# Kernel optimization log

Hardware: AMD Instinct MI355X
Metric: run time of the kernel (lower is better)

## Reference

```python
import jax, jax.numpy as jnp
import numpy as np

E = 128  # embedding_dim
C = 32   # per-head dim
H = 4    # heads
L = 256  # seq_len
N = 1    # batch


def layer_norm(x, gamma, beta, eps=1e-5):
    mu = jnp.mean(x, axis=-1, keepdims=True)
    var = jnp.mean((x - mu) ** 2, axis=-1, keepdims=True)
    return (x - mu) * jax.lax.rsqrt(var + eps) * gamma + beta


def setup_inputs() -> dict:
    key = jax.random.key(0)
    ks = jax.random.split(key, 12)
    s = E ** -0.5
    return {
        "pair_rep": jax.random.normal(ks[0], (N, L, L, E), dtype=jnp.float32),
        "mask": jax.random.normal(ks[1], (N, L, L), dtype=jnp.float32) * 0.1,
        "gamma": jnp.ones((E,), dtype=jnp.float32),
        "beta": jnp.zeros((E,), dtype=jnp.float32),
        "Wq": jax.random.normal(ks[2], (E, C * H), dtype=jnp.float32) * s,
        "Wk": jax.random.normal(ks[3], (E, C * H), dtype=jnp.float32) * s,
        "Wv": jax.random.normal(ks[4], (E, C * H), dtype=jnp.float32) * s,
        "Wb": jax.random.normal(ks[5], (E, H), dtype=jnp.float32) * s,
        "Wfu": jax.random.normal(ks[6], (E, C * H), dtype=jnp.float32) * s,
        "bfu": jnp.zeros((C * H,), dtype=jnp.float32),
        "Wo": jax.random.normal(ks[7], (C * H, E), dtype=jnp.float32) * (C * H) ** -0.5,
        "bo": jnp.zeros((E,), dtype=jnp.float32),
    }


def reference(pair_rep, mask, gamma, beta, Wq, Wk, Wv, Wb, Wfu, bfu, Wo, bo):
    n, s, _, _ = pair_rep.shape
    x = layer_norm(pair_rep, gamma, beta)  # [n,s,s,E]
    q = (x @ Wq).reshape(n, s, s, H, C) * (C ** -0.5)
    k = (x @ Wk).reshape(n, s, s, H, C)
    v = (x @ Wv).reshape(n, s, s, H, C)
    # faithful to original einsum: keys carry the q index, queries the v index
    dpa = jnp.einsum('nsqhc,nsvhc->nsqvh', k, q)  # [n,s,q,v,h]
    dpa = dpa + mask[:, None, :, :, None]
    pair_bias = x @ Wb  # [n,s,s,H]
    attn = jax.nn.softmax(dpa + pair_bias[:, None], axis=3)
    out = jnp.einsum('nsqvh,nsvhc->nsqhc', attn, v)  # [n,s,q,h,c]
    fu = jax.nn.sigmoid(x @ Wfu + bfu).reshape(n, s, s, H, C)
    out = out * fu
    out = out.reshape(n, s, s, H * C) @ Wo + bo
    return out
```

## Files before the change

### kernel.cpp

```cpp
#include <hip/hip_runtime.h>
#include <math.h>

#define L 256
#define E 128
#define H 4
#define C 32
#define P (L*L)

typedef __bf16 bf16;
typedef __bf16 bf16x8 __attribute__((ext_vector_type(8)));
typedef __bf16 bf16x4 __attribute__((ext_vector_type(4)));
typedef float  f32x4  __attribute__((ext_vector_type(4)));

#define MFMA(a,b,c) __builtin_amdgcn_mfma_f32_16x16x32_bf16((a),(b),(c),0,0,0)

__global__ __launch_bounds__(256) void k_prep(
    const float* __restrict__ Wq, const float* __restrict__ Wk,
    const float* __restrict__ Wv, const float* __restrict__ Wfu,
    const float* __restrict__ Wo, const float* __restrict__ Wb,
    bf16* __restrict__ WF, bf16* __restrict__ WoF, bf16* __restrict__ WbF)
{
  const int b = blockIdx.x;
  const int lane = threadIdx.x & 63, wv = threadIdx.x >> 6;
  const int g = lane >> 4, l15 = lane & 15;
  if (b < 40) {
    const int m = b >> 3;
    const int f = (b & 7) * 4 + wv;
    const float* W = (m==0)?Wq:(m==1)?Wk:(m==2)?Wv:(m==3)?Wfu:Wo;
    bf16* dst = (m < 4) ? (WF + (size_t)m * 16384) : WoF;
    const float sc = (m == 0) ? 0.17677669529663689f : 1.0f;
    const int mt = f >> 2, kt = f & 3;
    const int row = 16*mt + l15, k0 = 32*kt + 8*g;
    bf16x8 o;
    #pragma unroll
    for (int j = 0; j < 8; ++j) o[j] = (bf16)(W[(size_t)(k0+j)*128 + row] * sc);
    *(bf16x8*)(dst + ((size_t)f*64 + lane)*8) = o;
  } else {
    const int kt = wv, k0 = 32*kt + 8*g;
    bf16x8 o;
    #pragma unroll
    for (int j = 0; j < 8; ++j)
      o[j] = (l15 < 4) ? (bf16)Wb[(size_t)(k0+j)*4 + l15] : (bf16)0.0f;
    *(bf16x8*)(WbF + ((size_t)kt*64 + lane)*8) = o;
  }
}

__global__ __launch_bounds__(512) void k_ln_proj(
    const float* __restrict__ pr, const float* __restrict__ gamma,
    const float* __restrict__ beta, const float* __restrict__ bfu,
    const bf16* __restrict__ WF, const bf16* __restrict__ WbF,
    bf16* __restrict__ qbh, bf16* __restrict__ kbh, bf16* __restrict__ vbh,
    bf16* __restrict__ gfb, float* __restrict__ pbo)
{
  __shared__ bf16 xs[64 * 136];
  __shared__ bf16 stag[4][16 * 136];
  const int tid = threadIdx.x;
  const int base = blockIdx.x * 64;
  const int w = tid >> 6, lane = tid & 63, g = lane >> 4, l15 = lane & 15;
  const int m = w & 3, half = w >> 2;

  const bf16* WFw = WF + (size_t)m * 16384 + (size_t)half * 8192;
  f32x4 af[16];
  #pragma unroll
  for (int f = 0; f < 16; ++f)
    af[f] = *(const f32x4*)(WFw + ((size_t)f*64 + lane)*8);

  {
    const int pl = tid >> 3, sub = tid & 7;
    const float4* src = (const float4*)(pr + (size_t)(base + pl) * 128 + sub * 16);
    float4 r[4];
    float s = 0.f, ss = 0.f;
    #pragma unroll
    for (int j = 0; j < 4; ++j) {
      r[j] = src[j];
      s  += r[j].x + r[j].y + r[j].z + r[j].w;
      ss += r[j].x*r[j].x + r[j].y*r[j].y + r[j].z*r[j].z + r[j].w*r[j].w;
    }
    s  += __shfl_xor(s, 1, 8);  s  += __shfl_xor(s, 2, 8);  s  += __shfl_xor(s, 4, 8);
    ss += __shfl_xor(ss, 1, 8); ss += __shfl_xor(ss, 2, 8); ss += __shfl_xor(ss, 4, 8);
    const float mu   = s * 0.0078125f;
    const float var  = ss * 0.0078125f - mu * mu;
    const float rstd = rsqrtf(var + 1e-5f);
    const float4* g4 = (const float4*)(gamma + sub * 16);
    const float4* b4 = (const float4*)(beta + sub * 16);
    bf16* xr = xs + pl * 136 + sub * 16;
    #pragma unroll
    for (int i = 0; i < 2; ++i) {
      float4 r0 = r[2*i], r1 = r[2*i+1];
      float4 gg0 = g4[2*i], gg1 = g4[2*i+1], bb0 = b4[2*i], bb1 = b4[2*i+1];
      bf16x8 o;
      o[0] = (bf16)((r0.x - mu) * rstd * gg0.x + bb0.x);
      o[1] = (bf16)((r0.y - mu) * rstd * gg0.y + bb0.y);
      o[2] = (bf16)((r0.z - mu) * rstd * gg0.z + bb0.z);
      o[3] = (bf16)((r0.w - mu) * rstd * gg0.w + bb0.w);
      o[4] = (bf16)((r1.x - mu) * rstd * gg1.x + bb1.x);
      o[5] = (bf16)((r1.y - mu) * rstd * gg1.y + bb1.y);
      o[6] = (bf16)((r1.z - mu) * rstd * gg1.z + bb1.z);
      o[7] = (bf16)((r1.w - mu) * rstd * gg1.w + bb1.w);
      *(bf16x8*)(xr + 8 * i) = o;
    }
  }

  #pragma unroll
  for (int f = 0; f < 16; ++f)
    asm volatile("" : "+v"(af[f]));

  __syncthreads();

  const f32x4 z = {0.f, 0.f, 0.f, 0.f};

  if (w < 4) {
    f32x4 acc = z;
    #pragma unroll
    for (int kt = 0; kt < 4; ++kt) {
      bf16x8 a = *(const bf16x8*)(WbF + ((size_t)kt*64 + lane)*8);
      bf16x8 b = *(const bf16x8*)(xs + (16*w + l15)*136 + 32*kt + 8*g);
      acc = MFMA(a, b, acc);
    }
    if (g == 0)
      *(float4*)(pbo + (size_t)(base + 16*w + l15)*4) =
          make_float4(acc[0], acc[1], acc[2], acc[3]);
  }

  bf16* stw = stag[m];

  for (int nt = 0; nt < 4; ++nt) {
    bf16x8 bfr[4];
    #pragma unroll
    for (int kt = 0; kt < 4; ++kt)
      bfr[kt] = *(const bf16x8*)(xs + (16*nt + l15)*136 + 32*kt + 8*g);
    f32x4 acc[4];
    #pragma unroll
    for (int mtl = 0; mtl < 4; ++mtl) acc[mtl] = z;
    #pragma unroll
    for (int kt = 0; kt < 4; ++kt)
      #pragma unroll
      for (int mtl = 0; mtl < 4; ++mtl)
        acc[mtl] = MFMA(__builtin_bit_cast(bf16x8, af[mtl*4 + kt]), bfr[kt], acc[mtl]);

    #pragma unroll
    for (int mtl = 0; mtl < 4; ++mtl) {
      const int col = half*64 + 16*mtl + 4*g;
      f32x4 vv = acc[mtl];
      if (m == 3) {
        float4 bb = *(const float4*)(bfu + col);
        vv[0] = 1.f / (1.f + __expf(-(vv[0] + bb.x)));
        vv[1] = 1.f / (1.f + __expf(-(vv[1] + bb.y)));
        vv[2] = 1.f / (1.f + __expf(-(vv[2] + bb.z)));
        vv[3] = 1.f / (1.f + __expf(-(vv[3] + bb.w)));
      }
      bf16x4 o;
      o[0] = (bf16)vv[0]; o[1] = (bf16)vv[1]; o[2] = (bf16)vv[2]; o[3] = (bf16)vv[3];
      *(bf16x4*)(stw + l15*136 + col) = o;
    }

    #pragma unroll
    for (int i = 0; i < 2; ++i) {
      const int flat = i*512 + lane*8;
      const int p = flat >> 6, cf = half*64 + (flat & 63);
      bf16x8 val = *(const bf16x8*)(stw + p*136 + cf);
      if (m == 3) {
        *(bf16x8*)(gfb + ((size_t)(base + 16*nt + p))*128 + cf) = val;
      } else {
        bf16* dst = (m == 0) ? qbh : (m == 1) ? kbh : vbh;
        const int h = cf >> 5;
        *(bf16x8*)(dst + ((size_t)h*P + base + 16*nt + p)*32 + (cf & 31)) = val;
      }
    }
  }
}

__global__ __launch_bounds__(256) void k_bias(
    const float* __restrict__ mask, const float* __restrict__ pb,
    bf16* __restrict__ T5)
{
  const int q = blockIdx.x;
  const int v = threadIdx.x;
  const size_t qv = (size_t)q*256 + v;
  const float m = mask[qv];
  float4 p = *(const float4*)(pb + qv*4);
  T5[qv]            = (bf16)(m + p.x);
  T5[qv +   65536]  = (bf16)(m + p.y);
  T5[qv + 2*65536]  = (bf16)(m + p.z);
  T5[qv + 3*65536]  = (bf16)(m + p.w);
}

__global__ __launch_bounds__(512) void k_attn(
    const bf16* __restrict__ qbh, const bf16* __restrict__ kbh,
    const bf16* __restrict__ vbh, const bf16* __restrict__ T5,
    bf16* __restrict__ aob)
{
  __shared__ bf16 qs[256 * 40];
  __shared__ bf16 vT[32 * 264];
  const int tid = threadIdx.x;
  const int s = blockIdx.x >> 2, h = blockIdx.x & 3;
  const int rb = s * 256;
  const bf16* qh = qbh + (size_t)h * P * 32;
  const bf16* kh = kbh + (size_t)h * P * 32;
  const bf16* vh = vbh + (size_t)h * P * 32;
  const bf16* T5h = T5 + (size_t)h * 65536;

  const int w = tid >> 6, lane = tid & 63, g = lane >> 4, l15 = lane & 15;

  #pragma unroll
  for (int i = 0; i < 2; ++i) {
    const int flat = i*4096 + tid*8;
    const int pos = flat >> 5, cc = flat & 31;
    const int slot = (pos & 0xE3) | ((pos & 0x04) << 2) | ((pos & 0x18) >> 1);
    bf16x8 qv = *(const bf16x8*)(qh + ((size_t)rb + pos)*32 + cc);
    *(bf16x8*)(qs + slot*40 + cc) = qv;
    bf16x8 vv = *(const bf16x8*)(vh + ((size_t)rb + pos)*32 + cc);
    #pragma unroll
    for (int j = 0; j < 8; ++j) {
      const int row = cc + j;
      const int a = row >> 3;
      const int X = (a << 5) | ((a >> 1) << 4);
      vT[row*264 + (pos ^ X)] = vv[j];
    }
  }

  bf16x8 bq0 = *(const bf16x8*)(kh + ((size_t)rb + w*32 +      l15)*32 + 8*g);
  bf16x8 bq1 = *(const bf16x8*)(kh + ((size_t)rb + w*32 + 16 + l15)*32 + 8*g);

  __syncthreads();

  bf16x8 av[2][8];
  #pragma unroll
  for (int mt = 0; mt < 2; ++mt) {
    const int row = 16*mt + l15;
    const int a = row >> 3;
    const int X = (a << 5) | ((a >> 1) << 4);
    #pragma unroll
    for (int kt = 0; kt < 8; ++kt)
      av[mt][kt] = *(const bf16x8*)(vT + row*264 + ((32*kt + 8*g) ^ X));
  }

  bf16* aoh = aob + (size_t)h * P * 32;
  const f32x4 z = {0.f, 0.f, 0.f, 0.f};

  #pragma unroll
  for (int qt = 0; qt < 2; ++qt) {
    const int q = w*32 + qt*16 + l15;
    const bf16x8 bq = qt ? bq1 : bq0;
    const bf16* Trow = T5h + (size_t)q * 256 + 8*g;
    f32x4 o0a = z, o0b = z, o1a = z, o1b = z;
    float rs = 0.f;
    #pragma unroll
    for (int kt = 0; kt < 8; ++kt) {
      bf16x8 a0 = *(const bf16x8*)(qs + (16*(2*kt + 0) + l15)*40 + 8*g);
      bf16x8 a1 = *(const bf16x8*)(qs + (16*(2*kt + 1) + l15)*40 + 8*g);
      f32x4 s0 = MFMA(a0, bq, z);
      f32x4 s1 = MFMA(a1, bq, z);
      bf16x4 b0 = *(const bf16x4*)(Trow + 32*kt);
      bf16x4 b1 = *(const bf16x4*)(Trow + 32*kt + 4);
      bf16x8 pf;
      #pragma unroll
      for (int r = 0; r < 4; ++r) {
        float e0 = __expf(s0[r] + (float)b0[r]);
        float e1 = __expf(s1[r] + (float)b1[r]);
        pf[r]     = (bf16)e0;
        pf[4 + r] = (bf16)e1;
        rs += e0 + e1;
      }
      if (kt & 1) {
        o0b = MFMA(av[0][kt], pf, o0b);
        o1b = MFMA(av[1][kt], pf, o1b);
      } else {
        o0a = MFMA(av[0][kt], pf, o0a);
        o1a = MFMA(av[1][kt], pf, o1a);
      }
    }
    rs += __shfl_xor(rs, 16);
    rs += __shfl_xor(rs, 32);
    const float inv = 1.f / rs;
    bf16x4 p0, p1;
    #pragma unroll
    for (int r = 0; r < 4; ++r) {
      p0[r] = (bf16)((o0a[r] + o0b[r]) * inv);
      p1[r] = (bf16)((o1a[r] + o1b[r]) * inv);
    }
    bf16* dst = aoh + ((size_t)rb + q)*32;
    *(bf16x4*)(dst + 4*g)      = p0;
    *(bf16x4*)(dst + 16 + 4*g) = p1;
  }
}

__global__ __launch_bounds__(512) void k_gate_out(
    const bf16* __restrict__ aob, const bf16* __restrict__ gfb,
    const bf16* __restrict__ WoF, const float* __restrict__ bo,
    float* __restrict__ out)
{
  __shared__ bf16 gs[64 * 136];
  const int tid = threadIdx.x;
  const int base = blockIdx.x * 64;
  const int w = tid >> 6, lane = tid & 63, g = lane >> 4, l15 = lane & 15;

  f32x4 wf[4];
  #pragma unroll
  for (int kt = 0; kt < 4; ++kt)
    wf[kt] = *(const f32x4*)(WoF + ((size_t)(w*4 + kt)*64 + lane)*8);

  #pragma unroll
  for (int i = 0; i < 2; ++i) {
    const int flat = i*4096 + tid*8;
    const int pos = flat >> 7, c = flat & 127, h = c >> 5;
    bf16x8 a = *(const bf16x8*)(aob + ((size_t)h*P + base + pos)*32 + (c & 31));
    bf16x8 f = *(const bf16x8*)(gfb + ((size_t)(base + pos))*128 + c);
    bf16x8 o;
    #pragma unroll
    for (int j = 0; j < 8; ++j) o[j] = (bf16)((float)a[j] * (float)f[j]);
    *(bf16x8*)(gs + pos*136 + c) = o;
  }

  #pragma unroll
  for (int kt = 0; kt < 4; ++kt)
    asm volatile("" : "+v"(wf[kt]));

  __syncthreads();

  const f32x4 z = {0.f, 0.f, 0.f, 0.f};
  const int col = 16*w + 4*g;
  const float4 bb = *(const float4*)(bo + col);

  for (int nt = 0; nt < 4; ++nt) {
    bf16x8 bfr[4];
    #pragma unroll
    for (int kt = 0; kt < 4; ++kt)
      bfr[kt] = *(const bf16x8*)(gs + (16*nt + l15)*136 + 32*kt + 8*g);
    f32x4 a0 = z;
    #pragma unroll
    for (int kt = 0; kt < 4; ++kt)
      a0 = MFMA(__builtin_bit_cast(bf16x8, wf[kt]), bfr[kt], a0);
    const int pos = base + 16*nt + l15;
    *(float4*)(out + (size_t)pos*128 + col) =
        make_float4(a0[0] + bb.x, a0[1] + bb.y, a0[2] + bb.z, a0[3] + bb.w);
  }
}

extern "C" void kernel_launch(void* const* d_in, const int* in_sizes, int n_in,
                              void* d_out, int out_size, void* d_ws, size_t ws_size,
                              hipStream_t stream) {
  const float* pr    = (const float*)d_in[0];
  const float* mask  = (const float*)d_in[1];
  const float* gamma = (const float*)d_in[2];
  const float* beta  = (const float*)d_in[3];
  const float* Wq    = (const float*)d_in[4];
  const float* Wk    = (const float*)d_in[5];
  const float* Wv    = (const float*)d_in[6];
  const float* Wb    = (const float*)d_in[7];
  const float* Wfu   = (const float*)d_in[8];
  const float* bfu   = (const float*)d_in[9];
  const float* Wo    = (const float*)d_in[10];
  const float* bo    = (const float*)d_in[11];
  float* out = (float*)d_out;

  bf16* qbh = (bf16*)d_ws;
  bf16* kbh = qbh + (size_t)H * P * 32;
  bf16* vbh = kbh + (size_t)H * P * 32;
  bf16* gfb = vbh + (size_t)H * P * 32;
  bf16* aob = gfb + (size_t)P * 128;
  bf16* T5  = aob + (size_t)H * P * 32;
  bf16* WF  = T5  + (size_t)H * P;
  bf16* WoF = WF  + 4 * 16384;
  bf16* WbF = WoF + 16384;
  float* pb = (float*)(WbF + 2048);

  k_prep<<<41, 256, 0, stream>>>(Wq, Wk, Wv, Wfu, Wo, Wb, WF, WoF, WbF);
  k_ln_proj<<<1024, 512, 0, stream>>>(pr, gamma, beta, bfu, WF, WbF,
                                      qbh, kbh, vbh, gfb, pb);
  k_bias<<<256, 256, 0, stream>>>(mask, pb, T5);
  k_attn<<<1024, 512, 0, stream>>>(qbh, kbh, vbh, T5, aob);
  k_gate_out<<<1024, 512, 0, stream>>>(aob, gfb, WoF, bo, out);
}
```

Before: 164.4 us.

## Fuse attention with gating and output projection into one kernel

Merges the attention and gate/output-projection kernels. Each block now covers half the query rows of one s-row and loops over all four heads, writing gated results into shared memory before the Wo projection. This removes the global round-trip of the attention output and one kernel launch. In exchange, each block reloads Q and V for its s-row, which is redundant across the two halves, and runs the heads serially with extra barriers. The grid also shrinks from 1024 to 512 blocks, and the larger shared footprint may lower occupancy.

After: 165.8 us. About the same (+0.8%).

```diff
diff --git a/kernel.cpp b/kernel.cpp
--- a/kernel.cpp
+++ b/kernel.cpp
@@ -185,64 +185,56 @@
   T5[qv + 3*65536]  = (bf16)(m + p.w);
 }
 
-__global__ __launch_bounds__(512) void k_attn(
+__global__ __launch_bounds__(512) void k_attn_gate(
     const bf16* __restrict__ qbh, const bf16* __restrict__ kbh,
     const bf16* __restrict__ vbh, const bf16* __restrict__ T5,
-    bf16* __restrict__ aob)
+    const bf16* __restrict__ gfb, const bf16* __restrict__ WoF,
+    const float* __restrict__ bo, float* __restrict__ out)
 {
   __shared__ bf16 qs[256 * 40];
   __shared__ bf16 vT[32 * 264];
+  __shared__ bf16 gs[128 * 136];
   const int tid = threadIdx.x;
-  const int s = blockIdx.x >> 2, h = blockIdx.x & 3;
+  const int s = blockIdx.x >> 1, hf = blockIdx.x & 1;
   const int rb = s * 256;
-  const bf16* qh = qbh + (size_t)h * P * 32;
-  const bf16* kh = kbh + (size_t)h * P * 32;
-  const bf16* vh = vbh + (size_t)h * P * 32;
-  const bf16* T5h = T5 + (size_t)h * 65536;
-
   const int w = tid >> 6, lane = tid & 63, g = lane >> 4, l15 = lane & 15;
-
-  #pragma unroll
-  for (int i = 0; i < 2; ++i) {
-    const int flat = i*4096 + tid*8;
-    const int pos = flat >> 5, cc = flat & 31;
-    const int slot = (pos & 0xE3) | ((pos & 0x04) << 2) | ((pos & 0x18) >> 1);
-    bf16x8 qv = *(const bf16x8*)(qh + ((size_t)rb + pos)*32 + cc);
-    *(bf16x8*)(qs + slot*40 + cc) = qv;
-    bf16x8 vv = *(const bf16x8*)(vh + ((size_t)rb + pos)*32 + cc);
-    #pragma unroll
-    for (int j = 0; j < 8; ++j) {
-      const int row = cc + j;
-      const int a = row >> 3;
-      const int X = (a << 5) | ((a >> 1) << 4);
-      vT[row*264 + (pos ^ X)] = vv[j];
-    }
-  }
-
-  bf16x8 bq0 = *(const bf16x8*)(kh + ((size_t)rb + w*32 +      l15)*32 + 8*g);
-  bf16x8 bq1 = *(const bf16x8*)(kh + ((size_t)rb + w*32 + 16 + l15)*32 + 8*g);
-
-  __syncthreads();
-
-  bf16x8 av[2][8];
-  #pragma unroll
-  for (int mt = 0; mt < 2; ++mt) {
-    const int row = 16*mt + l15;
-    const int a = row >> 3;
-    const int X = (a << 5) | ((a >> 1) << 4);
-    #pragma unroll
-    for (int kt = 0; kt < 8; ++kt)
-      av[mt][kt] = *(const bf16x8*)(vT + row*264 + ((32*kt + 8*g) ^ X));
-  }
-
-  bf16* aoh = aob + (size_t)h * P * 32;
+  const int ql = hf*128 + w*16 + l15;
+
   const f32x4 z = {0.f, 0.f, 0.f, 0.f};
 
-  #pragma unroll
-  for (int qt = 0; qt < 2; ++qt) {
-    const int q = w*32 + qt*16 + l15;
-    const bf16x8 bq = qt ? bq1 : bq0;
-    const bf16* Trow = T5h + (size_t)q * 256 + 8*g;
+  for (int h = 0; h < 4; ++h) {
+    if (h) __syncthreads();
+
+    const bf16* qh = qbh + (size_t)h * P * 32;
+    const bf16* kh = kbh + (size_t)h * P * 32;
+    const bf16* vh = vbh + (size_t)h * P * 32;
+
+    bf16x8 bq = *(const bf16x8*)(kh + ((size_t)rb + ql)*32 + 8*g);
+
+    #pragma unroll
+    for (int i = 0; i < 2; ++i) {
+      const int flat = i*4096 + tid*8;
+      const int pos = flat >> 5, cc = flat & 31;
+      const int slot = (pos & 0xE3) | ((pos & 0x04) << 2) | ((pos & 0x18) >> 1);
+      bf16x8 qv = *(const bf16x8*)(qh + ((size_t)rb + pos)*32 + cc);
+      *(bf16x8*)(qs + slot*40 + cc) = qv;
+      bf16x8 vv = *(const bf16x8*)(vh + ((size_t)rb + pos)*32 + cc);
+      #pragma unroll
+      for (int j = 0; j < 8; ++j) {
+        const int row = cc + j;
+        const int a = row >> 3;
+        const int X = (a << 5) | ((a >> 1) << 4);
+        vT[row*264 + (pos ^ X)] = vv[j];
+      }
+    }
+    __syncthreads();
+
+    const int a0r = l15 >> 3;
+    const int X0 = (a0r << 5) | ((a0r >> 1) << 4);
+    const int a1r = (16 + l15) >> 3;
+    const int X1 = (a1r << 5) | ((a1r >> 1) << 4);
+
+    const bf16* Trow = T5 + (size_t)h * 65536 + (size_t)ql * 256 + 8*g;
     f32x4 o0a = z, o0b = z, o1a = z, o1b = z;
     float rs = 0.f;
     #pragma unroll
@@ -262,76 +254,57 @@
         pf[4 + r] = (bf16)e1;
         rs += e0 + e1;
       }
+      bf16x8 av0 = *(const bf16x8*)(vT + (l15)*264      + ((32*kt + 8*g) ^ X0));
+      bf16x8 av1 = *(const bf16x8*)(vT + (16 + l15)*264 + ((32*kt + 8*g) ^ X1));
       if (kt & 1) {
-        o0b = MFMA(av[0][kt], pf, o0b);
-        o1b = MFMA(av[1][kt], pf, o1b);
+        o0b = MFMA(av0, pf, o0b);
+        o1b = MFMA(av1, pf, o1b);
       } else {
-        o0a = MFMA(av[0][kt], pf, o0a);
-        o1a = MFMA(av[1][kt], pf, o1a);
+        o0a = MFMA(av0, pf, o0a);
+        o1a = MFMA(av1, pf, o1a);
       }
     }
     rs += __shfl_xor(rs, 16);
     rs += __shfl_xor(rs, 32);
     const float inv = 1.f / rs;
+
+    const bf16* grow = gfb + ((size_t)rb + ql)*128 + 32*h;
+    bf16x4 g0 = *(const bf16x4*)(grow + 4*g);
+    bf16x4 g1 = *(const bf16x4*)(grow + 16 + 4*g);
+
     bf16x4 p0, p1;
     #pragma unroll
     for (int r = 0; r < 4; ++r) {
-      p0[r] = (bf16)((o0a[r] + o0b[r]) * inv);
-      p1[r] = (bf16)((o1a[r] + o1b[r]) * inv);
-    }
-    bf16* dst = aoh + ((size_t)rb + q)*32;
-    *(bf16x4*)(dst + 4*g)      = p0;
-    *(bf16x4*)(dst + 16 + 4*g) = p1;
-  }
-}
-
-__global__ __launch_bounds__(512) void k_gate_out(
-    const bf16* __restrict__ aob, const bf16* __restrict__ gfb,
-    const bf16* __restrict__ WoF, const float* __restrict__ bo,
-    float* __restrict__ out)
-{
-  __shared__ bf16 gs[64 * 136];
-  const int tid = threadIdx.x;
-  const int base = blockIdx.x * 64;
-  const int w = tid >> 6, lane = tid & 63, g = lane >> 4, l15 = lane & 15;
+      p0[r] = (bf16)((o0a[r] + o0b[r]) * inv * (float)g0[r]);
+      p1[r] = (bf16)((o1a[r] + o1b[r]) * inv * (float)g1[r]);
+    }
+    bf16* gr = gs + (size_t)(w*16 + l15)*136 + 32*h;
+    *(bf16x4*)(gr + 4*g)      = p0;
+    *(bf16x4*)(gr + 16 + 4*g) = p1;
+  }
 
   f32x4 wf[4];
   #pragma unroll
   for (int kt = 0; kt < 4; ++kt)
     wf[kt] = *(const f32x4*)(WoF + ((size_t)(w*4 + kt)*64 + lane)*8);
-
-  #pragma unroll
-  for (int i = 0; i < 2; ++i) {
-    const int flat = i*4096 + tid*8;
-    const int pos = flat >> 7, c = flat & 127, h = c >> 5;
-    bf16x8 a = *(const bf16x8*)(aob + ((size_t)h*P + base + pos)*32 + (c & 31));
-    bf16x8 f = *(const bf16x8*)(gfb + ((size_t)(base + pos))*128 + c);
-    bf16x8 o;
-    #pragma unroll
-    for (int j = 0; j < 8; ++j) o[j] = (bf16)((float)a[j] * (float)f[j]);
-    *(bf16x8*)(gs + pos*136 + c) = o;
-  }
-
   #pragma unroll
   for (int kt = 0; kt < 4; ++kt)
     asm volatile("" : "+v"(wf[kt]));
 
   __syncthreads();
 
-  const f32x4 z = {0.f, 0.f, 0.f, 0.f};
   const int col = 16*w + 4*g;
   const float4 bb = *(const float4*)(bo + col);
-
-  for (int nt = 0; nt < 4; ++nt) {
+  for (int nt = 0; nt < 8; ++nt) {
     bf16x8 bfr[4];
     #pragma unroll
     for (int kt = 0; kt < 4; ++kt)
-      bfr[kt] = *(const bf16x8*)(gs + (16*nt + l15)*136 + 32*kt + 8*g);
+      bfr[kt] = *(const bf16x8*)(gs + (size_t)(16*nt + l15)*136 + 32*kt + 8*g);
     f32x4 a0 = z;
     #pragma unroll
     for (int kt = 0; kt < 4; ++kt)
       a0 = MFMA(__builtin_bit_cast(bf16x8, wf[kt]), bfr[kt], a0);
-    const int pos = base + 16*nt + l15;
+    const int pos = rb + hf*128 + 16*nt + l15;
     *(float4*)(out + (size_t)pos*128 + col) =
         make_float4(a0[0] + bb.x, a0[1] + bb.y, a0[2] + bb.z, a0[3] + bb.w);
   }
@@ -369,6 +342,5 @@
   k_ln_proj<<<1024, 512, 0, stream>>>(pr, gamma, beta, bfu, WF, WbF,
                                       qbh, kbh, vbh, gfb, pb);
   k_bias<<<256, 256, 0, stream>>>(mask, pb, T5);
-  k_attn<<<1024, 512, 0, stream>>>(qbh, kbh, vbh, T5, aob);
-  k_gate_out<<<1024, 512, 0, stream>>>(aob, gfb, WoF, bo, out);
-}
+  k_attn_gate<<<512, 512, 0, stream>>>(qbh, kbh, vbh, T5, gfb, WoF, bo, out);
+}
```
